# Performance work log

Hardware: AMD Instinct MI355X
Metric: run time of the kernel (lower is better)

Reference implementation:

```python
import jax, jax.numpy as jnp
import numpy as np

NUM_HEADS = 12

def setup_inputs() -> dict:
    key = jax.random.key(0)
    ks = jax.random.split(key, 8)
    B, N, C = 8, 1024, 768
    H = NUM_HEADS
    return {
        "x": jax.random.normal(ks[0], (B, N, C), dtype=jnp.float32),
        "relative_position_index": jax.random.randint(ks[1], (N, N), 0, 2048, dtype=jnp.int64),
        "qkv_weight": jax.random.normal(ks[2], (3 * C, C), dtype=jnp.float32) * 0.02,
        "q_bias": jax.random.normal(ks[3], (C,), dtype=jnp.float32) * 0.02,
        "v_bias": jax.random.normal(ks[4], (C,), dtype=jnp.float32) * 0.02,
        "proj_weight": jax.random.normal(ks[5], (C, C), dtype=jnp.float32) * 0.02,
        "proj_bias": jax.random.normal(ks[6], (C,), dtype=jnp.float32) * 0.02,
        "rel_pos_bias_table": jax.random.normal(ks[7], (2048, H), dtype=jnp.float32) * 0.02,
    }

def reference(x, relative_position_index, qkv_weight, q_bias, v_bias, proj_weight, proj_bias, rel_pos_bias_table):
    B, N, C = x.shape
    H = NUM_HEADS
    d = C // H
    scale = d ** (-0.5)
    # qkv bias: (q_bias, zeros, v_bias) as in the torch module
    qkv_b = jnp.concatenate([q_bias, jnp.zeros_like(v_bias), v_bias])
    qkv = x @ qkv_weight.T + qkv_b  # [B,N,3C]
    qkv = qkv.reshape(B, N, 3, H, d).transpose(2, 0, 3, 1, 4)  # [3,B,H,N,d]
    q, k, v = qkv[0], qkv[1], qkv[2]
    attn = jnp.einsum("bhnd,bhmd->bhnm", q * scale, k)  # [B,H,N,N]
    # relative position bias: table lookup [N,N,H] -> [H,N,N]
    bias = rel_pos_bias_table[relative_position_index].transpose(2, 0, 1)
    attn = attn + bias[None]
    attn = jax.nn.softmax(attn, axis=-1)
    out = jnp.einsum("bhnm,bhmd->bhnd", attn, v)  # [B,H,N,d]
    out = out.transpose(0, 2, 1, 3).reshape(B, N, C)
    return out @ proj_weight.T + proj_bias
```

## Files before the change

### kernel.cpp

```cpp
#include <hip/hip_runtime.h>

typedef unsigned short ushort_t;
typedef __bf16 bf16x8 __attribute__((ext_vector_type(8)));
typedef float f32x4 __attribute__((ext_vector_type(4)));
typedef unsigned int u32x4 __attribute__((ext_vector_type(4)));

#define MFMA(a, b, c) __builtin_amdgcn_mfma_f32_16x16x32_bf16((a), (b), (c), 0, 0, 0)

#define BATCH 8
#define SEQ 1024
#define CDIM 768
#define NH 12
#define HD 64
#define MTOT (BATCH * SEQ)
#define THREEC (3 * CDIM)
#define KVB 64
#define LOG2E 1.44269504088896f

__device__ __forceinline__ ushort_t f2bf(float f) {
    unsigned int u = __builtin_bit_cast(unsigned int, f);
    u = (u + 0x7FFFu + ((u >> 16) & 1u)) >> 16;
    return (ushort_t)u;
}
__device__ __forceinline__ float bf2f(ushort_t b) {
    unsigned int u = ((unsigned int)b) << 16;
    return __builtin_bit_cast(float, u);
}
__device__ __forceinline__ ushort_t bfbits(float f) {
    __bf16 h = (__bf16)f;
    return __builtin_bit_cast(ushort_t, h);
}
__device__ __forceinline__ unsigned int pack2bf(float a, float b) {
    ushort2 p;
    p.x = bfbits(a);
    p.y = bfbits(b);
    return __builtin_bit_cast(unsigned int, p);
}

typedef const __attribute__((address_space(1))) unsigned int* gas_ptr;
typedef __attribute__((address_space(3))) unsigned int* las_ptr;

__device__ __forceinline__ void async16(const ushort_t* g, ushort_t* l) {
    __builtin_amdgcn_global_load_lds((gas_ptr)(const void*)g, (las_ptr)(void*)l, 16, 0, 0);
}

#define WAITVM_(N) asm volatile("s_waitcnt vmcnt(" #N ")" ::: "memory")
#define WAITVM(N) WAITVM_(N)
#define SCHEDB __builtin_amdgcn_sched_barrier(0)

__global__ __launch_bounds__(256) void k_convert(const float* __restrict__ x,
                                                 const float* __restrict__ wq,
                                                 const float* __restrict__ wp,
                                                 ushort_t* __restrict__ xb,
                                                 ushort_t* __restrict__ wqb,
                                                 ushort_t* __restrict__ wpb) {
    const int NX = MTOT * CDIM / 4;
    const int NQ = THREEC * CDIM / 4;
    const int NP = CDIM * CDIM / 4;
    int i = blockIdx.x * 256 + threadIdx.x;
    const float4* src;
    ushort_t* dst;
    int off;
    if (i < NX) { src = (const float4*)x; dst = xb; off = i; }
    else if (i < NX + NQ) { src = (const float4*)wq; dst = wqb; off = i - NX; }
    else if (i < NX + NQ + NP) { src = (const float4*)wp; dst = wpb; off = i - NX - NQ; }
    else return;
    float4 v = src[off];
    ushort4 o;
    o.x = f2bf(v.x); o.y = f2bf(v.y); o.z = f2bf(v.z); o.w = f2bf(v.w);
    ((ushort4*)dst)[off] = o;
}

__global__ __launch_bounds__(256) void k_bias(const int* __restrict__ rpi,
                                              const float* __restrict__ table,
                                              ushort_t* __restrict__ biasF) {
    __shared__ int idx_s[16][64];
    int tr = blockIdx.x;
    int tcq = blockIdx.y;
    int t = threadIdx.x;
    {
        int r = t >> 4;
        int c4 = (t & 15) * 4;
        int4 v = *(const int4*)&rpi[(tr * 16 + r) * SEQ + tcq * 64 + c4];
        *(int4*)&idx_s[r][c4] = v;
    }
    __syncthreads();
    int j = t >> 6;
    int lane = t & 63;
    int lq = lane >> 4, l15 = lane & 15;
    int tc = tcq * 4 + j;
    int id[4];
#pragma unroll
    for (int rr = 0; rr < 4; rr++) id[rr] = idx_s[l15][j * 16 + lq * 4 + rr];
#pragma unroll
    for (int h = 0; h < NH; h++) {
        ushort4 o;
        o.x = f2bf(table[id[0] * NH + h] * LOG2E);
        o.y = f2bf(table[id[1] * NH + h] * LOG2E);
        o.z = f2bf(table[id[2] * NH + h] * LOG2E);
        o.w = f2bf(table[id[3] * NH + h] * LOG2E);
        *(ushort4*)&biasF[(((h * 64 + tr) * 64 + tc) * 256 + lane * 4)] = o;
    }
}

template <int MODE>
__global__ __launch_bounds__(256) void k_gemm(const ushort_t* __restrict__ A,
                                              const ushort_t* __restrict__ Bw,
                                              const float* __restrict__ biasq,
                                              const float* __restrict__ biasv,
                                              const float* __restrict__ biasp,
                                              ushort_t* __restrict__ qb,
                                              ushort_t* __restrict__ kb,
                                              ushort_t* __restrict__ vT,
                                              float* __restrict__ outp) {
    __shared__ __attribute__((aligned(16))) ushort_t As[128 * 64];
    __shared__ __attribute__((aligned(16))) ushort_t Bs[128 * 64];
    const int K = CDIM;
    int tid = threadIdx.x, wave = tid >> 6, lane = tid & 63;
    int l15 = lane & 15, lq = lane >> 4;
    int wm = wave >> 1, wn = wave & 1;
    int nx = gridDim.x;
    int bidl = blockIdx.y * nx + blockIdx.x;
    int chunk = (nx * gridDim.y) >> 3;
    int swz = (bidl & 7) * chunk + (bidl >> 3);
    int colBase = (swz % nx) * 128;
    int rowBase = (swz / nx) * 128;
    f32x4 acc[4][4] = {};
    int srow = wave * 8 + (lane >> 3);
    int scol = (((lane & 7) ^ (srow & 7))) * 8;
    int l7 = l15 & 7;
    for (int k0 = 0; k0 < K; k0 += 64) {
#pragma unroll
        for (int is = 0; is < 4; is++) {
            async16(A + (rowBase + is * 32 + srow) * K + k0 + scol,
                    As + is * 2048 + tid * 8);
            async16(Bw + (colBase + is * 32 + srow) * K + k0 + scol,
                    Bs + is * 2048 + tid * 8);
        }
        asm volatile("s_waitcnt vmcnt(0)" ::: "memory");
        __syncthreads();
#pragma unroll
        for (int kk = 0; kk < 64; kk += 32) {
            bf16x8 af[4], bfr[4];
#pragma unroll
            for (int mf = 0; mf < 4; mf++)
                af[mf] = *(const bf16x8*)&As[(wm * 64 + mf * 16 + l15) * 64 +
                                             ((((kk >> 3) + lq) ^ l7) * 8)];
#pragma unroll
            for (int nf = 0; nf < 4; nf++)
                bfr[nf] = *(const bf16x8*)&Bs[(wn * 64 + nf * 16 + l15) * 64 +
                                              ((((kk >> 3) + lq) ^ l7) * 8)];
#pragma unroll
            for (int mf = 0; mf < 4; mf++)
#pragma unroll
                for (int nf = 0; nf < 4; nf++)
                    acc[mf][nf] = MFMA(af[mf], bfr[nf], acc[mf][nf]);
        }
        __syncthreads();
    }
#pragma unroll
    for (int mf = 0; mf < 4; mf++) {
#pragma unroll
        for (int nf = 0; nf < 4; nf++) {
            int jc = colBase + wn * 64 + nf * 16 + l15;
            int mg0 = rowBase + wm * 64 + mf * 16 + (lane >> 4) * 4;
            if (MODE == 0) {
                int which = jc / CDIM;
                int co = jc - which * CDIM;
                int b = mg0 >> 10, tok0 = mg0 & 1023;
                int hh = co >> 6, dd = co & 63;
                int bh = b * NH + hh;
                if (which == 0) {
                    float bq_ = biasq[co];
#pragma unroll
                    for (int r = 0; r < 4; r++)
                        qb[(bh * SEQ + tok0 + r) * HD + dd] =
                            f2bf((acc[mf][nf][r] + bq_) * 0.125f);
                } else if (which == 1) {
#pragma unroll
                    for (int r = 0; r < 4; r++)
                        kb[(bh * SEQ + tok0 + r) * HD + dd] = f2bf(acc[mf][nf][r]);
                } else {
                    float bv = biasv[co];
                    ushort4 pk;
                    pk.x = f2bf(acc[mf][nf][0] + bv);
                    pk.y = f2bf(acc[mf][nf][1] + bv);
                    pk.z = f2bf(acc[mf][nf][2] + bv);
                    pk.w = f2bf(acc[mf][nf][3] + bv);
                    *(ushort4*)&vT[(size_t)(bh * HD + dd) * SEQ + tok0] = pk;
                }
            } else {
                float bp_ = biasp[jc];
#pragma unroll
                for (int r = 0; r < 4; r++)
                    outp[(size_t)(mg0 + r) * CDIM + jc] = acc[mf][nf][r] + bp_;
            }
        }
    }
}

__global__ __launch_bounds__(256, 4) void k_attn(const ushort_t* __restrict__ qb,
                                                 const ushort_t* __restrict__ kb,
                                                 const ushort_t* __restrict__ vT,
                                                 const ushort_t* __restrict__ biasF,
                                                 ushort_t* __restrict__ ctx) {
    __shared__ __attribute__((aligned(16))) ushort_t Ks[2][KVB * 64];
    __shared__ __attribute__((aligned(16))) ushort_t Vs[KVB * 64];

    int lin = ((int)blockIdx.x & 7) * 192 + ((int)blockIdx.x >> 3);
    int h = lin >> 7;
    int b = (lin >> 4) & 7;
    int qt = lin & 15;
    int bh = b * NH + h;
    int tid = threadIdx.x, w = tid >> 6, lane = tid & 63;
    int l15 = lane & 15, lq = lane >> 4, lq4 = lq * 4;
    int row0 = qt * 64 + w * 16;
    int qtile0 = row0 >> 4;

    const ushort_t* qp = qb + bh * SEQ * HD;
    const ushort_t* kp = kb + bh * SEQ * HD;
    const ushort_t* vp = vT + bh * HD * SEQ;
    const ushort_t* bfp = biasF + (size_t)(h * 64 + qtile0) * 64 * 256;

    int lamA = l15 + 32 * (lq & 1);
    int lamB = lamA + 16;

    int rk0, sk0, rk1, sk1;
    {
        int cid0 = tid;
        rk0 = cid0 >> 3; sk0 = ((cid0 & 7) ^ (rk0 & 7)) * 8;
        int cid1 = 256 + tid;
        rk1 = cid1 >> 3; sk1 = ((cid1 & 7) ^ (rk1 & 7)) * 8;
    }

#define STAGE_K(BUF, C0)                                                    \
    do {                                                                    \
        async16(kp + ((C0) + rk0) * HD + sk0, &Ks[BUF][tid * 8]);           \
        async16(kp + ((C0) + rk1) * HD + sk1, &Ks[BUF][(256 + tid) * 8]);   \
    } while (0)
#define STAGE_V(C0)                                                         \
    do {                                                                    \
        async16(vp + rk0 * SEQ + (C0) + sk0, &Vs[tid * 8]);                 \
        async16(vp + rk1 * SEQ + (C0) + sk1, &Vs[(256 + tid) * 8]);         \
    } while (0)

    STAGE_K(0, 0); STAGE_V(0); STAGE_K(1, KVB);

    bf16x8 qfr0 = *(const bf16x8*)&qp[(row0 + l15) * HD + 8 * lq];
    bf16x8 qfr1 = *(const bf16x8*)&qp[(row0 + l15) * HD + 32 + 8 * lq];

    f32x4 Oa[4] = {};
    float li = 0.0f;
    f32x4 accA[4], accB[4];
    unsigned int u0[4][2];

#define QK_BLOCK(AN, KN)                                                       \
    do {                                                                       \
        __builtin_amdgcn_s_setprio(1);                                         \
        _Pragma("unroll") for (int n = 0; n < 4; n++) {                        \
            int krow = n * 16 + l15;                                           \
            bf16x8 kf0 = *(const bf16x8*)&(KN)[krow * 64 + ((lq ^ (krow & 7)) * 8)]; \
            bf16x8 kf1 = *(const bf16x8*)&(KN)[krow * 64 + (((lq + 4) ^ (krow & 7)) * 8)]; \
            f32x4 z0 = {};                                                     \
            z0 = MFMA(kf0, qfr0, z0); z0 = MFMA(kf1, qfr1, z0);                \
            (AN)[n] = z0;                                                      \
        }                                                                      \
        __builtin_amdgcn_s_setprio(0);                                         \
    } while (0)

#define SOFTMAX_STEP(ACC)                                                      \
    do {                                                                       \
        f32x4 sv = {};                                                         \
        _Pragma("unroll") for (int n = 0; n < 4; n++) {                        \
            float p0 = exp2f(fmaf((ACC)[n][0], LOG2E, bf2f(bfr[n].x)));        \
            float p1 = exp2f(fmaf((ACC)[n][1], LOG2E, bf2f(bfr[n].y)));        \
            float p2 = exp2f(fmaf((ACC)[n][2], LOG2E, bf2f(bfr[n].z)));        \
            float p3 = exp2f(fmaf((ACC)[n][3], LOG2E, bf2f(bfr[n].w)));        \
            sv[0] += p0; sv[1] += p1; sv[2] += p2; sv[3] += p3;                \
            u0[n][0] = pack2bf(p0, p1);                                        \
            u0[n][1] = pack2bf(p2, p3);                                        \
        }                                                                      \
        li += (sv[0] + sv[1]) + (sv[2] + sv[3]);                               \
    } while (0)

#define ASSEMBLE(KS, PF)                                                       \
    do {                                                                       \
        unsigned int a0 = __shfl((int)u0[2 * (KS)][0], lamA);                  \
        unsigned int b0 = __shfl((int)u0[2 * (KS) + 1][0], lamA);              \
        unsigned int a1 = __shfl((int)u0[2 * (KS)][1], lamA);                  \
        unsigned int b1 = __shfl((int)u0[2 * (KS) + 1][1], lamA);              \
        unsigned int a2 = __shfl((int)u0[2 * (KS)][0], lamB);                  \
        unsigned int b2 = __shfl((int)u0[2 * (KS) + 1][0], lamB);              \
        unsigned int a3 = __shfl((int)u0[2 * (KS)][1], lamB);                  \
        unsigned int b3 = __shfl((int)u0[2 * (KS) + 1][1], lamB);              \
        bool hi_ = (lq & 2) != 0;                                              \
        u32x4 qd;                                                              \
        qd[0] = hi_ ? b0 : a0; qd[1] = hi_ ? b1 : a1;                          \
        qd[2] = hi_ ? b2 : a2; qd[3] = hi_ ? b3 : a3;                          \
        (PF) = __builtin_bit_cast(bf16x8, qd);                                 \
    } while (0)

#define PV_BLOCK()                                                             \
    do {                                                                       \
        __builtin_amdgcn_s_setprio(1);                                         \
        _Pragma("unroll") for (int ks = 0; ks < 2; ks++) {                     \
            bf16x8 pfa;                                                        \
            ASSEMBLE(ks, pfa);                                                 \
            _Pragma("unroll") for (int nc = 0; nc < 4; nc++) {                 \
                int vrow = nc * 16 + l15;                                      \
                bf16x8 vf = *(const bf16x8*)&Vs[vrow * 64 + (((ks * 4 + lq) ^ (vrow & 7)) * 8)]; \
                Oa[nc] = MFMA(pfa, vf, Oa[nc]);                                \
            }                                                                  \
        }                                                                      \
        __builtin_amdgcn_s_setprio(0);                                         \
    } while (0)

#define ITER(T, AC, AN, DO_KST, DO_VST, DO_QK)                                 \
    do {                                                                       \
        WAITVM(0);                                                             \
        SCHEDB;                                                                \
        __builtin_amdgcn_s_barrier();                                          \
        SCHEDB;                                                                \
        const int t_ = (T);                                                    \
        ushort4 bfr[4];                                                        \
        {                                                                      \
            int kt0 = t_ * 4;                                                  \
            _Pragma("unroll") for (int n = 0; n < 4; n++)                      \
                bfr[n] = *(const ushort4*)&bfp[(kt0 + n) * 256 + lane * 4];    \
        }                                                                      \
        if (DO_KST) STAGE_K(t_ & 1, (t_ + 2) * KVB);                           \
        if (DO_QK) QK_BLOCK(AN, Ks[(t_ + 1) & 1]);                             \
        SOFTMAX_STEP(AC);                                                      \
        PV_BLOCK();                                                            \
        if (DO_VST) {                                                          \
            SCHEDB;                                                            \
            __builtin_amdgcn_s_barrier();                                      \
            SCHEDB;                                                            \
            STAGE_V((t_ + 1) * KVB);                                           \
        }                                                                      \
    } while (0)

    WAITVM(2);
    SCHEDB;
    __builtin_amdgcn_s_barrier();
    SCHEDB;
    QK_BLOCK(accA, Ks[0]);

#pragma unroll 1
    for (int tt = 0; tt < 14; tt += 2) {
        ITER(tt,     accA, accB, 1, 1, 1);
        ITER(tt + 1, accB, accA, 1, 1, 1);
    }
    ITER(14, accA, accB, 0, 1, 1);
    ITER(15, accB, accA, 0, 0, 0);

    float lsum = li;
    lsum += __shfl_xor(lsum, 16);
    lsum += __shfl_xor(lsum, 32);
    float rli = 1.0f / lsum;
#pragma unroll
    for (int r = 0; r < 4; r++) {
        float rl = __shfl(rli, (lane & 48) | (lq4 + r));
#pragma unroll
        for (int nc = 0; nc < 4; nc++) {
            ctx[(size_t)(b * SEQ + row0 + lq4 + r) * CDIM + h * HD + nc * 16 + l15] =
                bfbits(Oa[nc][r] * rl);
        }
    }
#undef ITER
#undef PV_BLOCK
#undef ASSEMBLE
#undef SOFTMAX_STEP
#undef QK_BLOCK
#undef STAGE_V
#undef STAGE_K
}

extern "C" void kernel_launch(void* const* d_in, const int* in_sizes, int n_in,
                              void* d_out, int out_size, void* d_ws, size_t ws_size,
                              hipStream_t stream) {
    const float* x = (const float*)d_in[0];
    const int* rpi = (const int*)d_in[1];
    const float* wqkv = (const float*)d_in[2];
    const float* qbias = (const float*)d_in[3];
    const float* vbias = (const float*)d_in[4];
    const float* wproj = (const float*)d_in[5];
    const float* pbias = (const float*)d_in[6];
    const float* table = (const float*)d_in[7];
    float* out = (float*)d_out;

    char* ws = (char*)d_ws;
    ushort_t* xb    = (ushort_t*)(ws + 0);
    ushort_t* wqb   = (ushort_t*)(ws + 12582912);
    ushort_t* wpb   = (ushort_t*)(ws + 16121856);
    ushort_t* qbuf  = (ushort_t*)(ws + 17301504);
    ushort_t* kbuf  = (ushort_t*)(ws + 29884416);
    ushort_t* vTbuf = (ushort_t*)(ws + 42467328);
    ushort_t* ctx   = (ushort_t*)(ws + 55050240);
    ushort_t* biasF = (ushort_t*)(ws + 67633152);

    k_convert<<<8448, 256, 0, stream>>>(x, wqkv, wproj, xb, wqb, wpb);
    k_bias<<<dim3(64, 16), 256, 0, stream>>>(rpi, table, biasF);
    k_gemm<0><<<dim3(THREEC / 128, MTOT / 128), 256, 0, stream>>>(
        xb, wqb, qbias, vbias, nullptr, qbuf, kbuf, vTbuf, nullptr);
    k_attn<<<1536, 256, 0, stream>>>(qbuf, kbuf, vTbuf, biasF, ctx);
    k_gemm<1><<<dim3(CDIM / 128, MTOT / 128), 256, 0, stream>>>(
        ctx, wpb, nullptr, nullptr, pbias, nullptr, nullptr, nullptr, out);
}
```

Baseline: 162.7 us.

## Double-buffer V tiles and prefetch bias one iteration ahead in attention

The V shared-memory tile becomes double-buffered, so staging the next V tile can start at the top of each iteration instead of after a second barrier that followed PV. The relative-position bias fragments for the next tile are now loaded into alternating register sets one iteration early, so their global latency overlaps the QK and softmax work. This removes one block-wide barrier per iteration and hides the bias load latency. In exchange it uses 8 KB more LDS and extra registers per thread, which could lower occupancy under the 4-blocks-per-CU launch bound. The prologue also changes to wait on all outstanding loads (WAITVM(0)) where it previously waited with WAITVM(2).

```diff
diff --git a/kernel.cpp b/kernel.cpp
--- a/kernel.cpp
+++ b/kernel.cpp
@@ -205,7 +205,7 @@
                                                  const ushort_t* __restrict__ biasF,
                                                  ushort_t* __restrict__ ctx) {
     __shared__ __attribute__((aligned(16))) ushort_t Ks[2][KVB * 64];
-    __shared__ __attribute__((aligned(16))) ushort_t Vs[KVB * 64];
+    __shared__ __attribute__((aligned(16))) ushort_t Vs[2][KVB * 64];
 
     int lin = ((int)blockIdx.x & 7) * 192 + ((int)blockIdx.x >> 3);
     int h = lin >> 7;
@@ -238,13 +238,17 @@
         async16(kp + ((C0) + rk0) * HD + sk0, &Ks[BUF][tid * 8]);           \
         async16(kp + ((C0) + rk1) * HD + sk1, &Ks[BUF][(256 + tid) * 8]);   \
     } while (0)
-#define STAGE_V(C0)                                                         \
+#define STAGE_V(BUF, C0)                                                    \
     do {                                                                    \
-        async16(vp + rk0 * SEQ + (C0) + sk0, &Vs[tid * 8]);                 \
-        async16(vp + rk1 * SEQ + (C0) + sk1, &Vs[(256 + tid) * 8]);         \
-    } while (0)
-
-    STAGE_K(0, 0); STAGE_V(0); STAGE_K(1, KVB);
+        async16(vp + rk0 * SEQ + (C0) + sk0, &Vs[BUF][tid * 8]);            \
+        async16(vp + rk1 * SEQ + (C0) + sk1, &Vs[BUF][(256 + tid) * 8]);    \
+    } while (0)
+#define LOAD_BIAS(DST, T)                                                   \
+    do {                                                                    \
+        int kt0 = (T) * 4;                                                  \
+        _Pragma("unroll") for (int n = 0; n < 4; n++)                       \
+            (DST)[n] = *(const ushort4*)&bfp[(kt0 + n) * 256 + lane * 4];   \
+    } while (0)
 
     bf16x8 qfr0 = *(const bf16x8*)&qp[(row0 + l15) * HD + 8 * lq];
     bf16x8 qfr1 = *(const bf16x8*)&qp[(row0 + l15) * HD + 32 + 8 * lq];
@@ -252,6 +256,7 @@
     f32x4 Oa[4] = {};
     float li = 0.0f;
     f32x4 accA[4], accB[4];
+    ushort4 bfrP[4], bfrQ[4];
     unsigned int u0[4][2];
 
 #define QK_BLOCK(AN, KN)                                                       \
@@ -268,14 +273,14 @@
         __builtin_amdgcn_s_setprio(0);                                         \
     } while (0)
 
-#define SOFTMAX_STEP(ACC)                                                      \
+#define SOFTMAX_STEP(ACC, BFR)                                                 \
     do {                                                                       \
         f32x4 sv = {};                                                         \
         _Pragma("unroll") for (int n = 0; n < 4; n++) {                        \
-            float p0 = exp2f(fmaf((ACC)[n][0], LOG2E, bf2f(bfr[n].x)));        \
-            float p1 = exp2f(fmaf((ACC)[n][1], LOG2E, bf2f(bfr[n].y)));        \
-            float p2 = exp2f(fmaf((ACC)[n][2], LOG2E, bf2f(bfr[n].z)));        \
-            float p3 = exp2f(fmaf((ACC)[n][3], LOG2E, bf2f(bfr[n].w)));        \
+            float p0 = exp2f(fmaf((ACC)[n][0], LOG2E, bf2f((BFR)[n].x)));      \
+            float p1 = exp2f(fmaf((ACC)[n][1], LOG2E, bf2f((BFR)[n].y)));      \
+            float p2 = exp2f(fmaf((ACC)[n][2], LOG2E, bf2f((BFR)[n].z)));      \
+            float p3 = exp2f(fmaf((ACC)[n][3], LOG2E, bf2f((BFR)[n].w)));      \
             sv[0] += p0; sv[1] += p1; sv[2] += p2; sv[3] += p3;                \
             u0[n][0] = pack2bf(p0, p1);                                        \
             u0[n][1] = pack2bf(p2, p3);                                        \
@@ -300,7 +305,7 @@
         (PF) = __builtin_bit_cast(bf16x8, qd);                                 \
     } while (0)
 
-#define PV_BLOCK()                                                             \
+#define PV_BLOCK(VC)                                                           \
     do {                                                                       \
         __builtin_amdgcn_s_setprio(1);                                         \
         _Pragma("unroll") for (int ks = 0; ks < 2; ks++) {                     \
@@ -308,39 +313,33 @@
             ASSEMBLE(ks, pfa);                                                 \
             _Pragma("unroll") for (int nc = 0; nc < 4; nc++) {                 \
                 int vrow = nc * 16 + l15;                                      \
-                bf16x8 vf = *(const bf16x8*)&Vs[vrow * 64 + (((ks * 4 + lq) ^ (vrow & 7)) * 8)]; \
+                bf16x8 vf = *(const bf16x8*)&(VC)[vrow * 64 + (((ks * 4 + lq) ^ (vrow & 7)) * 8)]; \
                 Oa[nc] = MFMA(pfa, vf, Oa[nc]);                                \
             }                                                                  \
         }                                                                      \
         __builtin_amdgcn_s_setprio(0);                                         \
     } while (0)
 
-#define ITER(T, AC, AN, DO_KST, DO_VST, DO_QK)                                 \
+#define ITER(T, AC, AN, BC, BN, DO_KST, DO_VST, DO_QK)                         \
     do {                                                                       \
         WAITVM(0);                                                             \
         SCHEDB;                                                                \
         __builtin_amdgcn_s_barrier();                                          \
         SCHEDB;                                                                \
         const int t_ = (T);                                                    \
-        ushort4 bfr[4];                                                        \
-        {                                                                      \
-            int kt0 = t_ * 4;                                                  \
-            _Pragma("unroll") for (int n = 0; n < 4; n++)                      \
-                bfr[n] = *(const ushort4*)&bfp[(kt0 + n) * 256 + lane * 4];    \
-        }                                                                      \
         if (DO_KST) STAGE_K(t_ & 1, (t_ + 2) * KVB);                           \
+        if (DO_VST) STAGE_V((t_ + 1) & 1, (t_ + 1) * KVB);                     \
+        if (DO_QK) LOAD_BIAS(BN, t_ + 1);                                      \
         if (DO_QK) QK_BLOCK(AN, Ks[(t_ + 1) & 1]);                             \
-        SOFTMAX_STEP(AC);                                                      \
-        PV_BLOCK();                                                            \
-        if (DO_VST) {                                                          \
-            SCHEDB;                                                            \
-            __builtin_amdgcn_s_barrier();                                      \
-            SCHEDB;                                                            \
-            STAGE_V((t_ + 1) * KVB);                                           \
-        }                                                                      \
-    } while (0)
-
-    WAITVM(2);
+        SOFTMAX_STEP(AC, BC);                                                  \
+        PV_BLOCK(Vs[t_ & 1]);                                                  \
+    } while (0)
+
+    STAGE_K(0, 0);
+    STAGE_V(0, 0);
+    STAGE_K(1, KVB);
+    LOAD_BIAS(bfrP, 0);
+    WAITVM(0);
     SCHEDB;
     __builtin_amdgcn_s_barrier();
     SCHEDB;
@@ -348,11 +347,11 @@
 
 #pragma unroll 1
     for (int tt = 0; tt < 14; tt += 2) {
-        ITER(tt,     accA, accB, 1, 1, 1);
-        ITER(tt + 1, accB, accA, 1, 1, 1);
-    }
-    ITER(14, accA, accB, 0, 1, 1);
-    ITER(15, accB, accA, 0, 0, 0);
+        ITER(tt,     accA, accB, bfrP, bfrQ, 1, 1, 1);
+        ITER(tt + 1, accB, accA, bfrQ, bfrP, 1, 1, 1);
+    }
+    ITER(14, accA, accB, bfrP, bfrQ, 0, 1, 1);
+    ITER(15, accB, accA, bfrQ, bfrP, 0, 0, 0);
 
     float lsum = li;
     lsum += __shfl_xor(lsum, 16);
@@ -372,6 +371,7 @@
 #undef ASSEMBLE
 #undef SOFTMAX_STEP
 #undef QK_BLOCK
+#undef LOAD_BIAS
 #undef STAGE_V
 #undef STAGE_K
 }
```

New measurement: 160.9 us, median of 2. Within noise of the previous version (-1.1%).
